# Kernel tuning notes

Hardware: AMD Instinct MI355X
Metric: run time of the kernel (lower is better)

## Reference

```python
import jax, jax.numpy as jnp
import numpy as np

Q = 32          # latent position dim; state vs = [v, s] has dim 2Q
N = 131072      # batch of ODE states
H = 50          # BNN hidden width (n_hidden=50 in source)
STEPS = 16      # fixed-step Euler steps (dense time grid)
DT = 0.1        # dt default from forward()
LN_EPS = 1e-5


def setup_inputs() -> dict:
    key = jax.random.key(0)
    ks = jax.random.split(key, 6)
    d = 2 * Q
    # weights scaled by 1/sqrt(fan_in) so Euler integration stays stable
    return {
        "z0": jax.random.normal(ks[0], (N, d), jnp.float32),
        "logp0": jax.random.normal(ks[1], (N,), jnp.float32),
        "W1": jax.random.normal(ks[2], (d, H), jnp.float32) / np.sqrt(d).astype(np.float32),
        "b1": jnp.zeros((H,), jnp.float32),
        "g1": jnp.ones((H,), jnp.float32),
        "be1": jnp.zeros((H,), jnp.float32),
        "W2": jax.random.normal(ks[3], (H, H), jnp.float32) / np.sqrt(H).astype(np.float32),
        "b2": jnp.zeros((H,), jnp.float32),
        "g2": jnp.ones((H,), jnp.float32),
        "be2": jnp.zeros((H,), jnp.float32),
        "W3": jax.random.normal(ks[4], (H, Q), jnp.float32) / np.sqrt(H).astype(np.float32),
        "b3": jnp.zeros((Q,), jnp.float32),
    }


def _layernorm(x, g, b):
    m = jnp.mean(x, axis=-1, keepdims=True)
    v = jnp.mean((x - m) ** 2, axis=-1, keepdims=True)
    return (x - m) * jax.lax.rsqrt(v + LN_EPS) * g + b


def reference(z0, logp0, W1, b1, g1, be1, W2, b2, g2, be2, W3, b3):
    d = z0.shape[1]
    q = d // 2

    def f(vs):  # BNN dynamics: [N, 2q] -> [N, q]
        h = jax.nn.celu(_layernorm(vs @ W1 + b1, g1, be1))
        h = jax.nn.celu(_layernorm(h @ W2 + b2, g2, be2))
        return h @ W3 + b3

    basis = jnp.eye(q, d, dtype=z0.dtype)  # [q, 2q] unit tangents in the velocity block

    def rhs(vs):
        dv = f(vs)          # dv/dt = f(vs)
        ds = vs[:, :q]      # ds/dt = v
        dvs = jnp.concatenate([dv, ds], axis=1)
        # trace of d(dv)/d(v) via q forward-mode JVPs (fused analogue of the
        # per-dim torch.autograd.grad loop in ode2vae_rhs)
        def jvp_i(e):
            _, t = jax.jvp(f, (vs,), (jnp.broadcast_to(e, vs.shape),))
            return t  # [N, q]
        tang = jax.vmap(jvp_i)(basis)        # [q, N, q]
        tr = jnp.einsum("ini->n", tang)      # sum_i d(dv_i)/d(v_i)
        return dvs, -tr

    def step(carry, _):
        vs, lp = carry
        dvs, dlp = rhs(vs)
        vs2 = vs + DT * dvs
        lp2 = lp + DT * dlp
        return (vs2, lp2), (vs2, lp2)

    _, (zt, lp) = jax.lax.scan(step, (z0, logp0), None, length=STEPS)
    # [STEPS, N, 2q+1]: trajectory states with log-density appended
    return jnp.concatenate([zt, lp[..., None]], axis=-1)
```

## Files before the change

kernel.cpp:

```cpp
#include <hip/hip_runtime.h>
#include <hip/hip_fp16.h>

#define NPART 131072
#define QDIM 32
#define DDIM 64
#define HDIM 50
#define STEPS 16
#define DT 0.1f
#define LN_EPS 1e-5f
#define INV_H 0.02f
#define ODIM 65

#define WS_W1TH 0
#define WS_W2TH 1600
#define WS_UTH  3000
#define WS_MH   4400
#define WS_W3H  5800
#define WS_JV   6600
#define WS_HV   6800
#define WS_TOT  7000

#define SLOT_FLOATS (HDIM * 256)
#define LDS_FLOATS  (SLOT_FLOATS + WS_TOT)

typedef float f4a __attribute__((ext_vector_type(4)));
typedef float f4u __attribute__((ext_vector_type(4), aligned(4)));
typedef unsigned int u32;
typedef _Float16 h2f __attribute__((ext_vector_type(2)));

__device__ __forceinline__ h2f as_h2(u32 x) { h2f r; __builtin_memcpy(&r, &x, 4); return r; }
__device__ __forceinline__ u32 h2bits(float a, float b) {
    h2f p; p[0] = (_Float16)a; p[1] = (_Float16)b;
    u32 r; __builtin_memcpy(&r, &p, 4); return r;
}
__device__ __forceinline__ h2f mk_h2(float a, float b) {
    h2f p; p[0] = (_Float16)a; p[1] = (_Float16)b; return p;
}

#if __has_builtin(__builtin_amdgcn_fdot2)
#define FDOT2(a, b, c) __builtin_amdgcn_fdot2((a), (b), (c), false)
#else
#define FDOT2(a, b, c) ((float)(a)[0] * (float)(b)[0] + ((float)(a)[1] * (float)(b)[1] + (c)))
#endif

__device__ __forceinline__ float pack2h(float x, float t) {
    u32 r = h2bits(x, t); float f; __builtin_memcpy(&f, &r, 4); return f;
}
__device__ __forceinline__ void unpack_lo(float f, float& x) {
    u32 u; __builtin_memcpy(&u, &f, 4); h2f p = as_h2(u); x = (float)p[0];
}
__device__ __forceinline__ void unpack2h(float f, float& x, float& t) {
    u32 u; __builtin_memcpy(&u, &f, 4); h2f p = as_h2(u); x = (float)p[0]; t = (float)p[1];
}

__global__ void ode2vae_setup(const float* __restrict__ W1,
                              const float* __restrict__ W2,
                              const float* __restrict__ W3,
                              const float* __restrict__ b1, const float* __restrict__ g1,
                              const float* __restrict__ be1,
                              const float* __restrict__ b2, const float* __restrict__ g2,
                              const float* __restrict__ be2,
                              float* __restrict__ ws)
{
    const int tid = threadIdx.x;
    u32* wsu = (u32*)ws;
    for (int i = tid; i < WS_TOT; i += 256) wsu[i] = 0u;
    __syncthreads();
    for (int idx = tid; idx < HDIM * 32; idx += 256) {
        const int h = idx / 32, k = idx % 32;
        wsu[WS_W1TH + h * 32 + k] = h2bits(W1[(2 * k) * HDIM + h], W1[(2 * k + 1) * HDIM + h]);
    }
    for (int idx = tid; idx < HDIM * 25; idx += 256) {
        const int j = idx / 25, k = idx % 25;
        float w2p[2], up[2], mp[2];
        #pragma unroll
        for (int s_ = 0; s_ < 2; ++s_) {
            const int h = 2 * k + s_;
            float u = 0.f;
            #pragma unroll
            for (int i = 0; i < QDIM; ++i)
                u = fmaf(W1[i * HDIM + h], W3[j * QDIM + i], u);
            const float w2 = W2[h * HDIM + j];
            float rs = 0.f;
            for (int jj = 0; jj < HDIM; ++jj) rs += W2[h * HDIM + jj];
            w2p[s_] = w2; up[s_] = u; mp[s_] = u * (w2 - INV_H * rs);
        }
        wsu[WS_W2TH + j * 28 + k] = h2bits(w2p[0], w2p[1]);
        wsu[WS_UTH  + j * 28 + k] = h2bits(up[0], up[1]);
        wsu[WS_MH   + j * 28 + k] = h2bits(mp[0], mp[1]);
    }
    for (int idx = tid; idx < HDIM * 16; idx += 256) {
        const int j = idx / 16, k = idx % 16;
        wsu[WS_W3H + j * 16 + k] = h2bits(W3[j * QDIM + 2 * k], W3[j * QDIM + 2 * k + 1]);
    }
    if (tid < HDIM) {
        float acc = 0.f;
        #pragma unroll
        for (int i = 0; i < QDIM; ++i) {
            float rs1 = 0.f;
            for (int h = 0; h < HDIM; ++h) rs1 += W1[i * HDIM + h];
            acc = fmaf(rs1, W3[tid * QDIM + i], acc);
        }
        ws[WS_JV + tid * 4 + 0] = g2[tid];
        ws[WS_JV + tid * 4 + 1] = be2[tid];
        ws[WS_JV + tid * 4 + 2] = b2[tid];
        ws[WS_JV + tid * 4 + 3] = acc;
        ws[WS_HV + tid * 4 + 0] = b1[tid];
        ws[WS_HV + tid * 4 + 1] = g1[tid];
        ws[WS_HV + tid * 4 + 2] = be1[tid];
        ws[WS_HV + tid * 4 + 3] = 0.f;
    }
}

#define DOT56(res, rowp, P)                                           \
    {                                                                 \
        float q0 = 0.f, q1 = 0.f, q2 = 0.f, q3 = 0.f;                 \
        const uint4* R_ = (const uint4*)(rowp);                       \
        _Pragma("unroll")                                             \
        for (int c_ = 0; c_ < 7; ++c_) {                              \
            const uint4 u_ = R_[c_];                                  \
            q0 = FDOT2(as_h2(u_.x), (P)[4*c_ + 0], q0);               \
            q1 = FDOT2(as_h2(u_.y), (P)[4*c_ + 1], q1);               \
            q2 = FDOT2(as_h2(u_.z), (P)[4*c_ + 2], q2);               \
            q3 = FDOT2(as_h2(u_.w), (P)[4*c_ + 3], q3);               \
        }                                                             \
        res = (q0 + q1) + (q2 + q3);                                  \
    }

#define DOT56X2(resA, resB, rowp, PA, PB)                             \
    {                                                                 \
        float a0 = 0.f, a1_ = 0.f, b0_ = 0.f, b1_ = 0.f;              \
        const uint4* R_ = (const uint4*)(rowp);                       \
        _Pragma("unroll")                                             \
        for (int c_ = 0; c_ < 7; ++c_) {                              \
            const uint4 u_ = R_[c_];                                  \
            a0  = FDOT2(as_h2(u_.x), (PA)[4*c_ + 0], a0);             \
            b0_ = FDOT2(as_h2(u_.x), (PB)[4*c_ + 0], b0_);            \
            a1_ = FDOT2(as_h2(u_.y), (PA)[4*c_ + 1], a1_);            \
            b1_ = FDOT2(as_h2(u_.y), (PB)[4*c_ + 1], b1_);            \
            a0  = FDOT2(as_h2(u_.z), (PA)[4*c_ + 2], a0);             \
            b0_ = FDOT2(as_h2(u_.z), (PB)[4*c_ + 2], b0_);            \
            a1_ = FDOT2(as_h2(u_.w), (PA)[4*c_ + 3], a1_);            \
            b1_ = FDOT2(as_h2(u_.w), (PB)[4*c_ + 3], b1_);            \
        }                                                             \
        resA = a0 + a1_; resB = b0_ + b1_;                            \
    }

#define DOT64(res, rowp, P)                                           \
    {                                                                 \
        float q0 = 0.f, q1 = 0.f, q2 = 0.f, q3 = 0.f;                 \
        const uint4* R_ = (const uint4*)(rowp);                       \
        _Pragma("unroll")                                             \
        for (int c_ = 0; c_ < 8; ++c_) {                              \
            const uint4 u_ = R_[c_];                                  \
            q0 = FDOT2(as_h2(u_.x), (P)[4*c_ + 0], q0);               \
            q1 = FDOT2(as_h2(u_.y), (P)[4*c_ + 1], q1);               \
            q2 = FDOT2(as_h2(u_.z), (P)[4*c_ + 2], q2);               \
            q3 = FDOT2(as_h2(u_.w), (P)[4*c_ + 3], q3);               \
        }                                                             \
        res = (q0 + q1) + (q2 + q3);                                  \
    }

#define SAXPY56H(rowp, sh, D)                                         \
    {                                                                 \
        const uint4* R_ = (const uint4*)(rowp);                       \
        _Pragma("unroll")                                             \
        for (int c_ = 0; c_ < 7; ++c_) {                              \
            const uint4 u_ = R_[c_];                                  \
            (D)[4*c_ + 0] = as_h2(u_.x) * (sh) + (D)[4*c_ + 0];       \
            (D)[4*c_ + 1] = as_h2(u_.y) * (sh) + (D)[4*c_ + 1];       \
            (D)[4*c_ + 2] = as_h2(u_.z) * (sh) + (D)[4*c_ + 2];       \
            (D)[4*c_ + 3] = as_h2(u_.w) * (sh) + (D)[4*c_ + 3];       \
        }                                                             \
    }
#define SAXPY32H(rowp, sh, D)                                         \
    {                                                                 \
        const uint4* R_ = (const uint4*)(rowp);                       \
        _Pragma("unroll")                                             \
        for (int c_ = 0; c_ < 4; ++c_) {                              \
            const uint4 u_ = R_[c_];                                  \
            (D)[4*c_ + 0] = as_h2(u_.x) * (sh) + (D)[4*c_ + 0];       \
            (D)[4*c_ + 1] = as_h2(u_.y) * (sh) + (D)[4*c_ + 1];       \
            (D)[4*c_ + 2] = as_h2(u_.z) * (sh) + (D)[4*c_ + 2];       \
            (D)[4*c_ + 3] = as_h2(u_.w) * (sh) + (D)[4*c_ + 3];       \
        }                                                             \
    }

__global__ __launch_bounds__(256, 2)
void ode2vae_main(const float* __restrict__ z0, const float* __restrict__ logp0,
                  const float* __restrict__ b3,
                  const float* __restrict__ wsc,
                  float* out)
{
    __shared__ float lds[LDS_FLOATS];
    const int tid = threadIdx.x;
    const int n = blockIdx.x * 256 + tid;

    for (int i = tid; i < WS_TOT; i += 256)
        ((u32*)lds)[SLOT_FLOATS + i] = ((const u32*)wsc)[i];
    __syncthreads();

    float* const L = lds + tid;
    const u32* LW1TH = (const u32*)(lds + SLOT_FLOATS) + WS_W1TH;
    const u32* LW2TH = (const u32*)(lds + SLOT_FLOATS) + WS_W2TH;
    const u32* LUTH  = (const u32*)(lds + SLOT_FLOATS) + WS_UTH;
    const u32* LMH   = (const u32*)(lds + SLOT_FLOATS) + WS_MH;
    const u32* LW3H  = (const u32*)(lds + SLOT_FLOATS) + WS_W3H;
    const f4a* LJV   = (const f4a*)(lds + SLOT_FLOATS + WS_JV);
    const f4a* LHV   = (const f4a*)(lds + SLOT_FLOATS + WS_HV);

    float zq[QDIM];
    {
        const f4a* zp = (const f4a*)(z0 + (size_t)n * DDIM);
        #pragma unroll
        for (int k = 0; k < 8; ++k) {
            f4a v = zp[k];
            zq[4*k] = v[0]; zq[4*k+1] = v[1]; zq[4*k+2] = v[2]; zq[4*k+3] = v[3];
        }
    }
    float lp = logp0[n];

    for (int s = 0; s < STEPS; ++s) {
        float* const odst = out + ((size_t)s * NPART + (size_t)n) * ODIM;
        const float* const zsprev = (s == 0)
            ? (z0 + (size_t)n * DDIM + QDIM)
            : (out + ((size_t)(s - 1) * NPART + (size_t)n) * ODIM + QDIM);

        float zs[QDIM];
        #pragma unroll
        for (int k = 0; k < 8; ++k) {
            f4u v = *(const f4u*)(zsprev + 4 * k);
            zs[4*k] = v[0]; zs[4*k+1] = v[1]; zs[4*k+2] = v[2]; zs[4*k+3] = v[3];
        }
        h2f zp[32];
        #pragma unroll
        for (int k = 0; k < 16; ++k) zp[k] = mk_h2(zq[2*k], zq[2*k+1]);
        #pragma unroll
        for (int k = 0; k < 16; ++k) zp[16 + k] = mk_h2(zs[2*k], zs[2*k+1]);

        float m1a = 0.f, v1a = 0.f;
        #pragma unroll 1
        for (int h = 0; h < HDIM; ++h) {
            float a1h;
            DOT64(a1h, LW1TH + h * 32, zp);
            const f4a hv = LHV[h];
            a1h += hv[0];
            L[h * 256] = a1h;
            m1a += a1h;
            v1a = fmaf(a1h, a1h, v1a);
        }
        #pragma unroll
        for (int k = 0; k < QDIM; ++k) zs[k] = fmaf(DT, zq[k], zs[k]);
        #pragma unroll
        for (int k = 0; k < 8; ++k) {
            f4u v = {zs[4*k], zs[4*k+1], zs[4*k+2], zs[4*k+3]};
            *(f4u*)(odst + QDIM + 4 * k) = v;
        }
        const float m1 = m1a * INV_H;
        float var1 = v1a * INV_H - m1 * m1;
        var1 = var1 > 0.f ? var1 : 0.f;
        const float r1 = rsqrtf(var1 + LN_EPS);

        h2f xh1p[28], hhp[28];
        #pragma unroll
        for (int hp = 0; hp < 25; ++hp) {
            const float xa = (L[(2*hp) * 256] - m1) * r1;
            const float xb = (L[(2*hp + 1) * 256] - m1) * r1;
            const f4a hva = LHV[2*hp], hvb = LHV[2*hp + 1];
            const float ya = fmaf(xa, hva[1], hva[2]);
            const float yb = fmaf(xb, hvb[1], hvb[2]);
            const float ea = __expf(ya), eb = __expf(yb);
            const float ca = (ya > 0.f) ? ya : (ea - 1.f);
            const float cb = (yb > 0.f) ? yb : (eb - 1.f);
            xh1p[hp] = mk_h2(xa, xb);
            hhp[hp]  = mk_h2(ca, cb);
        }
        #pragma unroll
        for (int hp = 25; hp < 28; ++hp) { xh1p[hp] = mk_h2(0.f, 0.f); hhp[hp] = mk_h2(0.f, 0.f); }

        float m2a = 0.f, v2a = 0.f;
        #pragma unroll 1
        for (int j = 0; j < HDIM; ++j) {
            float a2j;
            DOT56(a2j, LW2TH + j * 28, hhp);
            const f4a jv = LJV[j];
            a2j += jv[2];
            L[j * 256] = a2j;
            m2a += a2j;
            v2a = fmaf(a2j, a2j, v2a);
        }
        const float m2 = m2a * INV_H;
        float var2 = v2a * INV_H - m2 * m2;
        var2 = var2 > 0.f ? var2 : 0.f;
        const float r2 = rsqrtf(var2 + LN_EPS);

        float suA = 0.f, syA = 0.f, tuA = 0.f, tyA = 0.f;
        #pragma unroll 1
        for (int j = 0; j < HDIM; ++j) {
            const float x2 = (L[j * 256] - m2) * r2;
            float t;
            DOT56(t, LUTH + j * 28, xh1p);
            const f4a jv = LJV[j];
            const float y = fmaf(x2, jv[0], jv[1]);
            const float e = __expf(y);
            const float w2vj = ((y > 0.f) ? 1.f : e) * (jv[0] * r2);
            const float tw = w2vj * t;
            L[j * 256] = pack2h(x2, tw);
            tuA += tw; tyA = fmaf(tw, x2, tyA);
            const float sw = jv[3] * w2vj;
            suA += sw; syA = fmaf(sw, x2, syA);
        }
        const float suH = suA * INV_H, syH = syA * INV_H;
        const float tuH = tuA * INV_H, tyH = tyA * INV_H;

        h2f w1vp[28], w1xp[28];
        #pragma unroll
        for (int hp = 0; hp < 25; ++hp) {
            const float xa = (float)xh1p[hp][0], xb = (float)xh1p[hp][1];
            const f4a hva = LHV[2*hp], hvb = LHV[2*hp + 1];
            const float ya = fmaf(xa, hva[1], hva[2]);
            const float yb = fmaf(xb, hvb[1], hvb[2]);
            const float ea = __expf(ya), eb = __expf(yb);
            const float wa = ((ya > 0.f) ? 1.f : ea) * (hva[1] * r1);
            const float wb = ((yb > 0.f) ? 1.f : eb) * (hvb[1] * r1);
            w1vp[hp] = mk_h2(wa, wb);
            w1xp[hp] = mk_h2(wa * xa, wb * xb);
        }
        #pragma unroll
        for (int hp = 25; hp < 28; ++hp) { w1vp[hp] = mk_h2(0.f, 0.f); w1xp[hp] = mk_h2(0.f, 0.f); }

        float S2 = 0.f, S3 = 0.f;
        #pragma unroll 1
        for (int j = 0; j < HDIM; ++j) {
            float x2, tw; unpack2h(L[j * 256], x2, tw);
            float cA_, cB_;
            DOT56X2(cA_, cB_, LW2TH + j * 28, w1vp, w1xp);
            const f4a jv = LJV[j];
            const float y = fmaf(x2, jv[0], jv[1]);
            const float e = __expf(y);
            const float w2vj = ((y > 0.f) ? 1.f : e) * (jv[0] * r2);
            const float q1 = fmaf(-syH, x2, jv[3] * w2vj - suH);
            const float q2 = fmaf(-tyH, x2, tw - tuH);
            S2 = fmaf(q1, cA_, S2);
            S3 = fmaf(q2, cB_, S3);
        }

        float T1A = 0.f;
        #pragma unroll 1
        for (int j = 0; j < HDIM; ++j) {
            float x2; unpack_lo(L[j * 256], x2);
            float cv;
            DOT56(cv, LMH + j * 28, w1vp);
            const f4a jv = LJV[j];
            const float y = fmaf(x2, jv[0], jv[1]);
            const float e = __expf(y);
            const float w2vj = ((y > 0.f) ? 1.f : e) * (jv[0] * r2);
            T1A = fmaf(w2vj, cv, T1A);
        }

        h2f duyp[28];
        #pragma unroll
        for (int k = 0; k < 28; ++k) duyp[k] = mk_h2(0.f, 0.f);
        #pragma unroll 1
        for (int j = 0; j < HDIM; ++j) {
            float x2; unpack_lo(L[j * 256], x2);
            const f4a jv = LJV[j];
            const float y = fmaf(x2, jv[0], jv[1]);
            const float e = __expf(y);
            const float w2vj = ((y > 0.f) ? 1.f : e) * (jv[0] * r2);
            const float y3 = x2 * w2vj;
            const h2f y3h = mk_h2(y3, y3);
            SAXPY56H(LUTH + j * 28, y3h, duyp);
        }
        #pragma unroll
        for (int k = 0; k < 28; ++k) duyp[k] = duyp[k] * w1vp[k];

        float T1c = 0.f;
        #pragma unroll 1
        for (int j = 0; j < HDIM; ++j) {
            float x2; unpack_lo(L[j * 256], x2);
            float cT;
            DOT56(cT, LW2TH + j * 28, duyp);
            T1c = fmaf(x2, cT, T1c);
        }
        const float tr = T1A - (T1c + S2 + S3) * INV_H;

        h2f dvp[16];
        #pragma unroll
        for (int k = 0; k < 16; ++k) dvp[k] = mk_h2(0.f, 0.f);
        #pragma unroll 1
        for (int j = 0; j < HDIM; ++j) {
            float x2; unpack_lo(L[j * 256], x2);
            const f4a jv = LJV[j];
            const float y = fmaf(x2, jv[0], jv[1]);
            const float e = __expf(y);
            const float h2v = (y > 0.f) ? y : (e - 1.f);
            const h2f hb = mk_h2(h2v, h2v);
            SAXPY32H(LW3H + j * 16, hb, dvp);
        }

        lp = fmaf(-DT, tr, lp);
        #pragma unroll
        for (int k = 0; k < 16; ++k) {
            const float da = (float)dvp[k][0] + b3[2*k];
            const float db = (float)dvp[k][1] + b3[2*k + 1];
            zq[2*k]     = fmaf(DT, da, zq[2*k]);
            zq[2*k + 1] = fmaf(DT, db, zq[2*k + 1]);
        }
        #pragma unroll
        for (int k = 0; k < 8; ++k) {
            f4u v = {zq[4*k], zq[4*k+1], zq[4*k+2], zq[4*k+3]};
            *(f4u*)(odst + 4 * k) = v;
        }
        odst[DDIM] = lp;
    }
}

extern "C" void kernel_launch(void* const* d_in, const int* in_sizes, int n_in,
                              void* d_out, int out_size, void* d_ws, size_t ws_size,
                              hipStream_t stream)
{
    const float* z0    = (const float*)d_in[0];
    const float* logp0 = (const float*)d_in[1];
    const float* W1    = (const float*)d_in[2];
    const float* b1    = (const float*)d_in[3];
    const float* g1    = (const float*)d_in[4];
    const float* be1   = (const float*)d_in[5];
    const float* W2    = (const float*)d_in[6];
    const float* b2    = (const float*)d_in[7];
    const float* g2    = (const float*)d_in[8];
    const float* be2   = (const float*)d_in[9];
    const float* W3    = (const float*)d_in[10];
    const float* b3    = (const float*)d_in[11];
    float* out = (float*)d_out;
    float* ws  = (float*)d_ws;

    hipLaunchKernelGGL(ode2vae_setup, dim3(1), dim3(256), 0, stream,
                       W1, W2, W3, b1, g1, be1, b2, g2, be2, ws);
    hipLaunchKernelGGL(ode2vae_main, dim3(NPART / 256), dim3(256), 0, stream,
                       z0, logp0, b3, ws, out);
}
```

Baseline: 1.578 ms.

## Fuse per-hidden-unit loops and switch dot products to packed half FMA

Merges the five separate loops over the 50 second-layer units into two passes. The duy SAXPY now shares the U row already loaded for the t dot product, and the S2/S3/T1c/T1A/dv loops share one pass with one exp per unit. The w1 derivative weights are computed in the first layer loop instead of a separate pass. Dot products now accumulate in packed fp16 (v_pk_fma) instead of fdot2 with fp32 accumulators, which cuts instruction count but lowers accumulation precision and keeps more live registers.

```diff
diff --git a/kernel.cpp b/kernel.cpp
--- a/kernel.cpp
+++ b/kernel.cpp
@@ -45,9 +45,6 @@
 
 __device__ __forceinline__ float pack2h(float x, float t) {
     u32 r = h2bits(x, t); float f; __builtin_memcpy(&f, &r, 4); return f;
-}
-__device__ __forceinline__ void unpack_lo(float f, float& x) {
-    u32 u; __builtin_memcpy(&u, &f, 4); h2f p = as_h2(u); x = (float)p[0];
 }
 __device__ __forceinline__ void unpack2h(float f, float& x, float& t) {
     u32 u; __builtin_memcpy(&u, &f, 4); h2f p = as_h2(u); x = (float)p[0]; t = (float)p[1];
@@ -112,6 +109,20 @@
     }
 }
 
+#define DOT64(res, rowp, P)                                           \
+    {                                                                 \
+        float q0 = 0.f, q1 = 0.f, q2 = 0.f, q3 = 0.f;                 \
+        const uint4* R_ = (const uint4*)(rowp);                       \
+        _Pragma("unroll")                                             \
+        for (int c_ = 0; c_ < 8; ++c_) {                              \
+            const uint4 u_ = R_[c_];                                  \
+            q0 = FDOT2(as_h2(u_.x), (P)[4*c_ + 0], q0);               \
+            q1 = FDOT2(as_h2(u_.y), (P)[4*c_ + 1], q1);               \
+            q2 = FDOT2(as_h2(u_.z), (P)[4*c_ + 2], q2);               \
+            q3 = FDOT2(as_h2(u_.w), (P)[4*c_ + 3], q3);               \
+        }                                                             \
+        res = (q0 + q1) + (q2 + q3);                                  \
+    }
 #define DOT56(res, rowp, P)                                           \
     {                                                                 \
         float q0 = 0.f, q1 = 0.f, q2 = 0.f, q3 = 0.f;                 \
@@ -127,62 +138,68 @@
         res = (q0 + q1) + (q2 + q3);                                  \
     }
 
-#define DOT56X2(resA, resB, rowp, PA, PB)                             \
-    {                                                                 \
-        float a0 = 0.f, a1_ = 0.f, b0_ = 0.f, b1_ = 0.f;              \
-        const uint4* R_ = (const uint4*)(rowp);                       \
+#define LDROW7(RB, SRC) { const uint4* S_ = (const uint4*)(SRC);      \
+    _Pragma("unroll") for (int c_ = 0; c_ < 7; ++c_) RB[c_] = S_[c_]; }
+#define LDROW4(RB, SRC) { const uint4* S_ = (const uint4*)(SRC);      \
+    _Pragma("unroll") for (int c_ = 0; c_ < 4; ++c_) RB[c_] = S_[c_]; }
+
+#define PKDOT_RB(res, RB, P)                                          \
+    {                                                                 \
+        h2f a0 = mk_h2(0.f, 0.f), a1_ = a0;                           \
         _Pragma("unroll")                                             \
         for (int c_ = 0; c_ < 7; ++c_) {                              \
-            const uint4 u_ = R_[c_];                                  \
-            a0  = FDOT2(as_h2(u_.x), (PA)[4*c_ + 0], a0);             \
-            b0_ = FDOT2(as_h2(u_.x), (PB)[4*c_ + 0], b0_);            \
-            a1_ = FDOT2(as_h2(u_.y), (PA)[4*c_ + 1], a1_);            \
-            b1_ = FDOT2(as_h2(u_.y), (PB)[4*c_ + 1], b1_);            \
-            a0  = FDOT2(as_h2(u_.z), (PA)[4*c_ + 2], a0);             \
-            b0_ = FDOT2(as_h2(u_.z), (PB)[4*c_ + 2], b0_);            \
-            a1_ = FDOT2(as_h2(u_.w), (PA)[4*c_ + 3], a1_);            \
-            b1_ = FDOT2(as_h2(u_.w), (PB)[4*c_ + 3], b1_);            \
-        }                                                             \
-        resA = a0 + a1_; resB = b0_ + b1_;                            \
-    }
-
-#define DOT64(res, rowp, P)                                           \
-    {                                                                 \
-        float q0 = 0.f, q1 = 0.f, q2 = 0.f, q3 = 0.f;                 \
-        const uint4* R_ = (const uint4*)(rowp);                       \
-        _Pragma("unroll")                                             \
-        for (int c_ = 0; c_ < 8; ++c_) {                              \
-            const uint4 u_ = R_[c_];                                  \
-            q0 = FDOT2(as_h2(u_.x), (P)[4*c_ + 0], q0);               \
-            q1 = FDOT2(as_h2(u_.y), (P)[4*c_ + 1], q1);               \
-            q2 = FDOT2(as_h2(u_.z), (P)[4*c_ + 2], q2);               \
-            q3 = FDOT2(as_h2(u_.w), (P)[4*c_ + 3], q3);               \
-        }                                                             \
-        res = (q0 + q1) + (q2 + q3);                                  \
-    }
-
-#define SAXPY56H(rowp, sh, D)                                         \
-    {                                                                 \
-        const uint4* R_ = (const uint4*)(rowp);                       \
+            a0  = as_h2(RB[c_].x) * (P)[4*c_ + 0] + a0;               \
+            a1_ = as_h2(RB[c_].y) * (P)[4*c_ + 1] + a1_;              \
+            a0  = as_h2(RB[c_].z) * (P)[4*c_ + 2] + a0;               \
+            a1_ = as_h2(RB[c_].w) * (P)[4*c_ + 3] + a1_;              \
+        }                                                             \
+        a0 = a0 + a1_;                                                \
+        res = (float)a0[0] + (float)a0[1];                            \
+    }
+
+#define PK3DOT_RB(rA, rB, rC, RB, PA, PB, PC)                         \
+    {                                                                 \
+        h2f aA = mk_h2(0.f, 0.f), aB = aA, aC = aA;                   \
         _Pragma("unroll")                                             \
         for (int c_ = 0; c_ < 7; ++c_) {                              \
-            const uint4 u_ = R_[c_];                                  \
-            (D)[4*c_ + 0] = as_h2(u_.x) * (sh) + (D)[4*c_ + 0];       \
-            (D)[4*c_ + 1] = as_h2(u_.y) * (sh) + (D)[4*c_ + 1];       \
-            (D)[4*c_ + 2] = as_h2(u_.z) * (sh) + (D)[4*c_ + 2];       \
-            (D)[4*c_ + 3] = as_h2(u_.w) * (sh) + (D)[4*c_ + 3];       \
-        }                                                             \
-    }
-#define SAXPY32H(rowp, sh, D)                                         \
-    {                                                                 \
-        const uint4* R_ = (const uint4*)(rowp);                       \
+            const h2f x_ = as_h2(RB[c_].x), y_ = as_h2(RB[c_].y);     \
+            const h2f z_ = as_h2(RB[c_].z), w_ = as_h2(RB[c_].w);     \
+            aA = x_ * (PA)[4*c_ + 0] + aA;                            \
+            aB = x_ * (PB)[4*c_ + 0] + aB;                            \
+            aC = x_ * (PC)[4*c_ + 0] + aC;                            \
+            aA = y_ * (PA)[4*c_ + 1] + aA;                            \
+            aB = y_ * (PB)[4*c_ + 1] + aB;                            \
+            aC = y_ * (PC)[4*c_ + 1] + aC;                            \
+            aA = z_ * (PA)[4*c_ + 2] + aA;                            \
+            aB = z_ * (PB)[4*c_ + 2] + aB;                            \
+            aC = z_ * (PC)[4*c_ + 2] + aC;                            \
+            aA = w_ * (PA)[4*c_ + 3] + aA;                            \
+            aB = w_ * (PB)[4*c_ + 3] + aB;                            \
+            aC = w_ * (PC)[4*c_ + 3] + aC;                            \
+        }                                                             \
+        rA = (float)aA[0] + (float)aA[1];                             \
+        rB = (float)aB[0] + (float)aB[1];                             \
+        rC = (float)aC[0] + (float)aC[1];                             \
+    }
+
+#define SAXPY_RB7(RB, sh, D)                                          \
+    {                                                                 \
+        _Pragma("unroll")                                             \
+        for (int c_ = 0; c_ < 7; ++c_) {                              \
+            (D)[4*c_ + 0] = as_h2(RB[c_].x) * (sh) + (D)[4*c_ + 0];   \
+            (D)[4*c_ + 1] = as_h2(RB[c_].y) * (sh) + (D)[4*c_ + 1];   \
+            (D)[4*c_ + 2] = as_h2(RB[c_].z) * (sh) + (D)[4*c_ + 2];   \
+            (D)[4*c_ + 3] = as_h2(RB[c_].w) * (sh) + (D)[4*c_ + 3];   \
+        }                                                             \
+    }
+#define SAXPY_RB4(RB, sh, D)                                          \
+    {                                                                 \
         _Pragma("unroll")                                             \
         for (int c_ = 0; c_ < 4; ++c_) {                              \
-            const uint4 u_ = R_[c_];                                  \
-            (D)[4*c_ + 0] = as_h2(u_.x) * (sh) + (D)[4*c_ + 0];       \
-            (D)[4*c_ + 1] = as_h2(u_.y) * (sh) + (D)[4*c_ + 1];       \
-            (D)[4*c_ + 2] = as_h2(u_.z) * (sh) + (D)[4*c_ + 2];       \
-            (D)[4*c_ + 3] = as_h2(u_.w) * (sh) + (D)[4*c_ + 3];       \
+            (D)[4*c_ + 0] = as_h2(RB[c_].x) * (sh) + (D)[4*c_ + 0];   \
+            (D)[4*c_ + 1] = as_h2(RB[c_].y) * (sh) + (D)[4*c_ + 1];   \
+            (D)[4*c_ + 2] = as_h2(RB[c_].z) * (sh) + (D)[4*c_ + 2];   \
+            (D)[4*c_ + 3] = as_h2(RB[c_].w) * (sh) + (D)[4*c_ + 3];   \
         }                                                             \
     }
 
@@ -261,7 +278,7 @@
         var1 = var1 > 0.f ? var1 : 0.f;
         const float r1 = rsqrtf(var1 + LN_EPS);
 
-        h2f xh1p[28], hhp[28];
+        h2f xh1p[28], hhp[28], w1vp[28], w1xp[28];
         #pragma unroll
         for (int hp = 0; hp < 25; ++hp) {
             const float xa = (L[(2*hp) * 256] - m1) * r1;
@@ -272,11 +289,18 @@
             const float ea = __expf(ya), eb = __expf(yb);
             const float ca = (ya > 0.f) ? ya : (ea - 1.f);
             const float cb = (yb > 0.f) ? yb : (eb - 1.f);
+            const float wa = ((ya > 0.f) ? 1.f : ea) * (hva[1] * r1);
+            const float wb = ((yb > 0.f) ? 1.f : eb) * (hvb[1] * r1);
             xh1p[hp] = mk_h2(xa, xb);
             hhp[hp]  = mk_h2(ca, cb);
-        }
-        #pragma unroll
-        for (int hp = 25; hp < 28; ++hp) { xh1p[hp] = mk_h2(0.f, 0.f); hhp[hp] = mk_h2(0.f, 0.f); }
+            w1vp[hp] = mk_h2(wa, wb);
+            w1xp[hp] = mk_h2(wa * xa, wb * xb);
+        }
+        #pragma unroll
+        for (int hp = 25; hp < 28; ++hp) {
+            xh1p[hp] = mk_h2(0.f, 0.f); hhp[hp] = mk_h2(0.f, 0.f);
+            w1vp[hp] = mk_h2(0.f, 0.f); w1xp[hp] = mk_h2(0.f, 0.f);
+        }
 
         float m2a = 0.f, v2a = 0.f;
         #pragma unroll 1
@@ -294,17 +318,25 @@
         var2 = var2 > 0.f ? var2 : 0.f;
         const float r2 = rsqrtf(var2 + LN_EPS);
 
+        h2f duyp[28];
+        #pragma unroll
+        for (int k = 0; k < 28; ++k) duyp[k] = mk_h2(0.f, 0.f);
         float suA = 0.f, syA = 0.f, tuA = 0.f, tyA = 0.f;
         #pragma unroll 1
         for (int j = 0; j < HDIM; ++j) {
+            uint4 RB[7];
+            LDROW7(RB, LUTH + j * 28);
             const float x2 = (L[j * 256] - m2) * r2;
-            float t;
-            DOT56(t, LUTH + j * 28, xh1p);
             const f4a jv = LJV[j];
             const float y = fmaf(x2, jv[0], jv[1]);
             const float e = __expf(y);
             const float w2vj = ((y > 0.f) ? 1.f : e) * (jv[0] * r2);
+            float t;
+            PKDOT_RB(t, RB, xh1p);
             const float tw = w2vj * t;
+            const float y3 = x2 * w2vj;
+            const h2f y3h = mk_h2(y3, y3);
+            SAXPY_RB7(RB, y3h, duyp);
             L[j * 256] = pack2h(x2, tw);
             tuA += tw; tyA = fmaf(tw, x2, tyA);
             const float sw = jv[3] * w2vj;
@@ -313,91 +345,40 @@
         const float suH = suA * INV_H, syH = syA * INV_H;
         const float tuH = tuA * INV_H, tyH = tyA * INV_H;
 
-        h2f w1vp[28], w1xp[28];
-        #pragma unroll
-        for (int hp = 0; hp < 25; ++hp) {
-            const float xa = (float)xh1p[hp][0], xb = (float)xh1p[hp][1];
-            const f4a hva = LHV[2*hp], hvb = LHV[2*hp + 1];
-            const float ya = fmaf(xa, hva[1], hva[2]);
-            const float yb = fmaf(xb, hvb[1], hvb[2]);
-            const float ea = __expf(ya), eb = __expf(yb);
-            const float wa = ((ya > 0.f) ? 1.f : ea) * (hva[1] * r1);
-            const float wb = ((yb > 0.f) ? 1.f : eb) * (hvb[1] * r1);
-            w1vp[hp] = mk_h2(wa, wb);
-            w1xp[hp] = mk_h2(wa * xa, wb * xb);
-        }
-        #pragma unroll
-        for (int hp = 25; hp < 28; ++hp) { w1vp[hp] = mk_h2(0.f, 0.f); w1xp[hp] = mk_h2(0.f, 0.f); }
-
-        float S2 = 0.f, S3 = 0.f;
+        #pragma unroll
+        for (int k = 0; k < 28; ++k) duyp[k] = duyp[k] * w1vp[k];
+
+        float S2 = 0.f, S3 = 0.f, T1c = 0.f, T1A = 0.f;
+        h2f dvp[16];
+        #pragma unroll
+        for (int k = 0; k < 16; ++k) dvp[k] = mk_h2(0.f, 0.f);
         #pragma unroll 1
         for (int j = 0; j < HDIM; ++j) {
             float x2, tw; unpack2h(L[j * 256], x2, tw);
-            float cA_, cB_;
-            DOT56X2(cA_, cB_, LW2TH + j * 28, w1vp, w1xp);
             const f4a jv = LJV[j];
             const float y = fmaf(x2, jv[0], jv[1]);
             const float e = __expf(y);
             const float w2vj = ((y > 0.f) ? 1.f : e) * (jv[0] * r2);
+            const float h2v = (y > 0.f) ? y : (e - 1.f);
             const float q1 = fmaf(-syH, x2, jv[3] * w2vj - suH);
             const float q2 = fmaf(-tyH, x2, tw - tuH);
-            S2 = fmaf(q1, cA_, S2);
-            S3 = fmaf(q2, cB_, S3);
-        }
-
-        float T1A = 0.f;
-        #pragma unroll 1
-        for (int j = 0; j < HDIM; ++j) {
-            float x2; unpack_lo(L[j * 256], x2);
-            float cv;
-            DOT56(cv, LMH + j * 28, w1vp);
-            const f4a jv = LJV[j];
-            const float y = fmaf(x2, jv[0], jv[1]);
-            const float e = __expf(y);
-            const float w2vj = ((y > 0.f) ? 1.f : e) * (jv[0] * r2);
-            T1A = fmaf(w2vj, cv, T1A);
-        }
-
-        h2f duyp[28];
-        #pragma unroll
-        for (int k = 0; k < 28; ++k) duyp[k] = mk_h2(0.f, 0.f);
-        #pragma unroll 1
-        for (int j = 0; j < HDIM; ++j) {
-            float x2; unpack_lo(L[j * 256], x2);
-            const f4a jv = LJV[j];
-            const float y = fmaf(x2, jv[0], jv[1]);
-            const float e = __expf(y);
-            const float w2vj = ((y > 0.f) ? 1.f : e) * (jv[0] * r2);
-            const float y3 = x2 * w2vj;
-            const h2f y3h = mk_h2(y3, y3);
-            SAXPY56H(LUTH + j * 28, y3h, duyp);
-        }
-        #pragma unroll
-        for (int k = 0; k < 28; ++k) duyp[k] = duyp[k] * w1vp[k];
-
-        float T1c = 0.f;
-        #pragma unroll 1
-        for (int j = 0; j < HDIM; ++j) {
-            float x2; unpack_lo(L[j * 256], x2);
-            float cT;
-            DOT56(cT, LW2TH + j * 28, duyp);
-            T1c = fmaf(x2, cT, T1c);
+            uint4 RB[7];
+            LDROW7(RB, LW2TH + j * 28);
+            float cS2, cS3, cTc;
+            PK3DOT_RB(cS2, cS3, cTc, RB, w1vp, w1xp, duyp);
+            LDROW7(RB, LMH + j * 28);
+            float cTA;
+            PKDOT_RB(cTA, RB, w1vp);
+            uint4 RB4[4];
+            LDROW4(RB4, LW3H + j * 16);
+            const h2f hb = mk_h2(h2v, h2v);
+            SAXPY_RB4(RB4, hb, dvp);
+            S2  = fmaf(q1, cS2, S2);
+            S3  = fmaf(q2, cS3, S3);
+            T1c = fmaf(x2, cTc, T1c);
+            T1A = fmaf(w2vj, cTA, T1A);
         }
         const float tr = T1A - (T1c + S2 + S3) * INV_H;
-
-        h2f dvp[16];
-        #pragma unroll
-        for (int k = 0; k < 16; ++k) dvp[k] = mk_h2(0.f, 0.f);
-        #pragma unroll 1
-        for (int j = 0; j < HDIM; ++j) {
-            float x2; unpack_lo(L[j * 256], x2);
-            const f4a jv = LJV[j];
-            const float y = fmaf(x2, jv[0], jv[1]);
-            const float e = __expf(y);
-            const float h2v = (y > 0.f) ? y : (e - 1.f);
-            const h2f hb = mk_h2(h2v, h2v);
-            SAXPY32H(LW3H + j * 16, hb, dvp);
-        }
 
         lp = fmaf(-DT, tr, lp);
         #pragma unroll
```

Result: faster. 1.438 ms (-8.9%).
